# Optimization experiments

Measured on AMD Instinct MI355X. Metric: run time of the kernel, lower is better.

Reference implementation:

```python
import jax, jax.numpy as jnp
import numpy as np

N_WAY, K_SHOT = 5, 1
N_CLASSES = 64
D = 8


def _conv(x, w, b):
    y = jax.lax.conv_general_dilated(x, w, (2, 2), 'SAME',
                                     dimension_numbers=('NCHW', 'OIHW', 'NCHW'))
    return jax.nn.relu(y + b[None, :, None, None])


def setup_inputs() -> dict:
    key = jax.random.key(0)
    ks = jax.random.split(key, 12)
    b, s_sup, q, h, w = 4, N_WAY * K_SHOT, 1, 64, 64
    rnd = lambda k, shape: jax.random.normal(k, shape, jnp.float32) * 0.05
    return {
        'support_x': jax.random.normal(ks[0], (b, s_sup, 3, h, w), jnp.float32),
        'support_y': jax.random.randint(ks[1], (b, s_sup), 0, N_CLASSES),
        'query_x': jax.random.normal(ks[2], (b, q, 3, h, w), jnp.float32),
        'query_y': jax.random.randint(ks[3], (b, q), 0, N_CLASSES),
        'k1': rnd(ks[4], (32, 3, 3, 3)), 'bc1': jnp.zeros((32,), jnp.float32),
        'k2': rnd(ks[5], (48, 32, 3, 3)), 'bc2': jnp.zeros((48,), jnp.float32),
        'k3': rnd(ks[6], (64, 48, 3, 3)), 'bc3': jnp.zeros((64,), jnp.float32),
        'Wlog': rnd(ks[7], (64, N_CLASSES)), 'blog': jnp.zeros((N_CLASSES,), jnp.float32),
        'Wg1': rnd(ks[8], (132, 128)), 'bg1': jnp.zeros((128,), jnp.float32),
        'Wg2': rnd(ks[9], (128, 64)), 'bg2': jnp.zeros((64,), jnp.float32),
        'Wf1': rnd(ks[10], (64, 16)), 'bf1': jnp.zeros((16,), jnp.float32),
        'Wf2': rnd(ks[11], (16, 1)), 'bf2': jnp.zeros((1,), jnp.float32),
    }


def reference(support_x, support_y, query_x, query_y,
              k1, bc1, k2, bc2, k3, bc3, Wlog, blog,
              Wg1, bg1, Wg2, bg2, Wf1, bf1, Wf2, bf2):
    x = jnp.concatenate([support_x, query_x], axis=1)       # [b, s, 3, h, w]
    label = jnp.concatenate([support_y, query_y], axis=1)   # [b, s]
    b, s = label.shape
    h, w = x.shape[-2:]

    feat = x.reshape(b * s, 3, h, w)
    feat = _conv(feat, k1, bc1)
    feat = _conv(feat, k2, bc2)
    feat = _conv(feat, k3, bc3)                              # [b*s, c, D, D]
    c = feat.shape[1]
    logits = feat.mean(axis=(2, 3)) @ Wlog + blog            # [b*s, n_classes]

    # --- append normalized (i/d, j/d) coord channels ---
    ii = jnp.arange(D, dtype=feat.dtype) / D
    coord = jnp.stack([jnp.broadcast_to(ii[:, None], (D, D)),
                       jnp.broadcast_to(ii[None, :], (D, D))])        # [2, D, D]
    feat = feat.reshape(b, s, c, D, D)
    feat = jnp.concatenate([feat, jnp.broadcast_to(coord, (b, s, 2, D, D))], axis=2)
    c2 = c + 2
    m = D * D
    a = feat.reshape(b, s, c2, m).transpose(0, 1, 3, 2)      # [b, s, m, c2]

    # --- relation network g over all (set-pair, position-pair) combos ---
    # original: g(concat(x_i, x_j)) where x_i = x[b, j, :, q], x_j = x[b, i, :, p]
    # split first linear: concat @ Wg1 = x_i @ Wg1[:c2] + x_j @ Wg1[c2:]
    W1a, W1b = Wg1[:c2], Wg1[c2:]
    u = a @ W1a                                              # [b, s_j, m_q, 128]
    v = a @ W1b + bg1                                        # [b, s_i, m_p, 128]
    # hdd[b,i,j,q,p] = relu(u[b,j,q] + v[b,i,p])  -> [b, s, s, m, m, 128]
    hdd = jax.nn.relu(u[:, None, :, :, None, :] + v[:, :, None, None, :, :])
    g = jax.nn.relu(hdd @ Wg2 + bg2)                         # [b, s, s, m, m, 64]
    x_f = g.sum(axis=(3, 4))                                 # [b, s, s, 64]
    score = jax.nn.sigmoid(jax.nn.relu(x_f @ Wf1 + bf1) @ Wf2 + bf2)  # [b, s, s, 1]

    # --- losses ---
    logp = jax.nn.log_softmax(logits, axis=-1)
    lab = label.reshape(-1)
    cls_loss = -jnp.take_along_axis(logp, lab[:, None], axis=1).mean()

    y = (label[:, :, None] == label[:, None, :])[..., None].astype(score.dtype)
    P = score[..., 0]                                        # [b, s, s]
    Pt = P.transpose(0, 2, 1)
    sym, anti = 0.5 * (P + Pt), 0.5 * (P - Pt)
    sym_n = jnp.sqrt((sym ** 2).sum(axis=(1, 2)))            # Frobenius per batch
    anti_n = jnp.sqrt((anti ** 2).sum(axis=(1, 2)))
    sym_loss = ((sym_n - anti_n) / (sym_n + anti_n)).mean()
    euc_loss = ((score - y) ** 2).mean()
    rn_loss = euc_loss - 0.1 * sym_loss
    return (cls_loss, rn_loss, sym_loss)
```

## Files before the change

kernel.cpp:

```cpp
#include <hip/hip_runtime.h>

typedef _Float16 f16x8 __attribute__((ext_vector_type(8)));
typedef float f32x4 __attribute__((ext_vector_type(4)));


__global__ void conv1_k(const float* __restrict__ sx, const float* __restrict__ qx,
                        const float* __restrict__ w, const float* __restrict__ bias,
                        float* __restrict__ out,
                        const float* __restrict__ Wg2, _Float16* __restrict__ W2h) {
    if (blockIdx.x == 768) {
        for (int s = 0; s < 4; s++) {
            int slot = threadIdx.x + 256*s;
            int tile = slot >> 6, lane = slot & 63;
            int kt = tile >> 2, nt = tile & 3;
            int quad = lane >> 4, col = lane & 15;
            f16x8 t;
            #pragma unroll
            for (int jj = 0; jj < 8; jj++)
                t[jj] = (_Float16)Wg2[(kt*32 + quad*8 + jj)*64 + nt*16 + col];
            *(f16x8*)&W2h[slot*8] = t;
        }
        return;
    }
    int r8 = blockIdx.x & 7, q = blockIdx.x >> 3;
    int n  = (q >> 5)*8 + r8;
    int oc = q & 31;
    int bi = n / 6, si = n % 6;
    const float* inp = (si < 5) ? sx + (size_t)((bi*5+si)*3)*4096
                                : qx + (size_t)(bi*3)*4096;
    __shared__ float wl[27];
    __shared__ float bl;
    if (threadIdx.x < 27) wl[threadIdx.x] = w[oc*27 + threadIdx.x];
    if (threadIdx.x == 0) bl = bias[oc];
    __syncthreads();
    for (int idx = threadIdx.x; idx < 1024; idx += 256) {
        int oy = idx >> 5, ox = idx & 31;
        float acc = bl;
        #pragma unroll
        for (int ic = 0; ic < 3; ic++) {
            const float* ip = inp + ic*4096;
            #pragma unroll
            for (int dy = 0; dy < 3; dy++) {
                int iy = 2*oy + dy;
                if (iy >= 64) continue;
                #pragma unroll
                for (int dx = 0; dx < 3; dx++) {
                    int ix = 2*ox + dx;
                    if (ix >= 64) continue;
                    acc += ip[iy*64+ix] * wl[ic*9 + dy*3 + dx];
                }
            }
        }
        out[(size_t)(n*32+oc)*1024 + idx] = fmaxf(acc, 0.f);
    }
}

__global__ void conv2_k(const float* __restrict__ in, const float* __restrict__ w,
                        const float* __restrict__ bias, float* __restrict__ out) {
    int r8 = blockIdx.x & 7, q = blockIdx.x >> 3;
    int n   = (q / 12)*8 + r8;
    int ocg = q % 12;
    __shared__ float wl[1152];
    __shared__ float pin[3][33*32];
    const int tid = threadIdx.x;
    for (int e = tid; e < 1152; e += 256) wl[e] = w[ocg*1152 + e];
    const float* ib = in + (size_t)n*32*1024;
    int srow = (tid*4) >> 5, scol = (tid*4) & 31;
    {
        f32x4 t0 = *(const f32x4*)&ib[tid*4];
        float* d = &pin[0][srow*33 + scol];
        d[0]=t0[0]; d[1]=t0[1]; d[2]=t0[2]; d[3]=t0[3];
    }
    f32x4 t1 = *(const f32x4*)&ib[1024 + tid*4];
    __syncthreads();
    int oy = tid >> 4, ox = tid & 15;
    float a0 = bias[ocg*4+0], a1 = bias[ocg*4+1];
    float a2 = bias[ocg*4+2], a3 = bias[ocg*4+3];
    for (int ic = 0; ic < 32; ic++) {
        f32x4 t2 = t1;
        if (ic + 2 < 32) t2 = *(const f32x4*)&ib[(size_t)(ic+2)*1024 + tid*4];
        const float* pp = pin[ic % 3];
        float tap[9];
        #pragma unroll
        for (int dy = 0; dy < 3; dy++)
            #pragma unroll
            for (int dx = 0; dx < 3; dx++) {
                int iy = 2*oy+dy, ix = 2*ox+dx;
                tap[dy*3+dx] = (iy < 32 && ix < 32) ? pp[iy*33 + ix] : 0.f;
            }
        #pragma unroll
        for (int t = 0; t < 9; t++) {
            a0 += tap[t]*wl[0*288 + ic*9 + t];
            a1 += tap[t]*wl[1*288 + ic*9 + t];
            a2 += tap[t]*wl[2*288 + ic*9 + t];
            a3 += tap[t]*wl[3*288 + ic*9 + t];
        }
        if (ic + 1 < 32) {
            float* d = &pin[(ic+1) % 3][srow*33 + scol];
            d[0]=t1[0]; d[1]=t1[1]; d[2]=t1[2]; d[3]=t1[3];
        }
        t1 = t2;
        __syncthreads();
    }
    size_t ob = (size_t)(n*48 + ocg*4)*256 + tid;
    out[ob        ] = fmaxf(a0, 0.f);
    out[ob + 256  ] = fmaxf(a1, 0.f);
    out[ob + 512  ] = fmaxf(a2, 0.f);
    out[ob + 768  ] = fmaxf(a3, 0.f);
}

__global__ void conv3_k(const float* __restrict__ in, const float* __restrict__ w,
                        const float* __restrict__ bias, float* __restrict__ out,
                        float* __restrict__ mf) {
    int r8 = blockIdx.x & 7, q = blockIdx.x >> 3;
    int n   = (q >> 3)*8 + r8;
    int ocg = q & 7;
    __shared__ float wl[3456];
    __shared__ float pin[3][17*16];
    const int tid = threadIdx.x;
    for (int e = tid; e < 3456; e += 256) wl[e] = w[ocg*3456 + e];
    const float* ib = in + (size_t)n*48*256;
    int srow = tid >> 4, scol = tid & 15;
    pin[0][srow*17 + scol] = ib[tid];
    float t1 = ib[256 + tid];
    __syncthreads();
    int pix = tid & 63, osub = tid >> 6;
    int oy = pix >> 3, ox = pix & 7;
    int ol0 = osub*2;
    float a0 = bias[ocg*8 + ol0], a1 = bias[ocg*8 + ol0 + 1];
    for (int ic = 0; ic < 48; ic++) {
        float t2 = t1;
        if (ic + 2 < 48) t2 = ib[(size_t)(ic+2)*256 + tid];
        const float* pp = pin[ic % 3];
        float tap[9];
        #pragma unroll
        for (int dy = 0; dy < 3; dy++)
            #pragma unroll
            for (int dx = 0; dx < 3; dx++) {
                int iy = 2*oy+dy, ix = 2*ox+dx;
                tap[dy*3+dx] = (iy < 16 && ix < 16) ? pp[iy*17 + ix] : 0.f;
            }
        #pragma unroll
        for (int t = 0; t < 9; t++) {
            a0 += tap[t]*wl[ ol0   *432 + ic*9 + t];
            a1 += tap[t]*wl[(ol0+1)*432 + ic*9 + t];
        }
        if (ic + 1 < 48) pin[(ic+1) % 3][srow*17 + scol] = t1;
        t1 = t2;
        __syncthreads();
    }
    float r0 = fmaxf(a0, 0.f), r1 = fmaxf(a1, 0.f);
    out[(size_t)(n*64 + ocg*8 + ol0  )*64 + pix] = r0;
    out[(size_t)(n*64 + ocg*8 + ol0+1)*64 + pix] = r1;
    #pragma unroll
    for (int off = 32; off >= 1; off >>= 1) {
        r0 += __shfl_xor(r0, off, 64);
        r1 += __shfl_xor(r1, off, 64);
    }
    if (pix == 0) {
        mf[n*64 + ocg*8 + ol0    ] = r0 * (1.f/64.f);
        mf[n*64 + ocg*8 + ol0 + 1] = r1 * (1.f/64.f);
    }
}

__global__ void uvcls_k(const float* __restrict__ feat3, const float* __restrict__ Wg1,
                        const float* __restrict__ bg1, _Float16* __restrict__ u,
                        _Float16* __restrict__ v,
                        const float* __restrict__ mf, const int* __restrict__ sy,
                        const int* __restrict__ qy, const float* __restrict__ Wlog,
                        const float* __restrict__ blog, float* __restrict__ rv) {
    int tid = threadIdx.x;
    if (blockIdx.x >= 384) {
        int n = blockIdx.x - 384;
        if (tid >= 64) return;
        int lane = tid;
        float s = blog[lane];
        for (int c = 0; c < 64; c++) s += mf[n*64 + c] * Wlog[c*64 + lane];
        float mx = s;
        #pragma unroll
        for (int off = 32; off >= 1; off >>= 1) mx = fmaxf(mx, __shfl_xor(mx, off, 64));
        float p = __expf(s - mx);
        float se = p;
        #pragma unroll
        for (int off = 32; off >= 1; off >>= 1) se += __shfl_xor(se, off, 64);
        int bi = n/6, si = n%6;
        int lab = (si < 5) ? sy[bi*5+si] : qy[bi];
        float s_lab = __shfl(s, lab, 64);
        if (lane == 0) rv[n] = -(s_lab - mx - __logf(se));
        return;
    }
    int r8 = blockIdx.x & 7, q = blockIdx.x >> 3;
    int bs = (q >> 4)*8 + r8;
    int pg = q & 15;
    __shared__ float a4[4][66];
    for (int e = tid; e < 264; e += 128) {
        int pl = e / 66, c = e % 66;
        int p = pg*4 + pl;
        float vv;
        if (c < 64)       vv = feat3[(size_t)(bs*64 + c)*64 + p];
        else if (c == 64) vv = (float)(p >> 3) * 0.125f;
        else              vv = (float)(p & 7) * 0.125f;
        a4[pl][c] = vv;
    }
    __syncthreads();
    float us[4] = {0.f,0.f,0.f,0.f};
    float bg = bg1[tid];
    float vs[4] = {bg,bg,bg,bg};
    for (int c = 0; c < 66; c++) {
        float wa = Wg1[c*128 + tid];
        float wb = Wg1[(66+c)*128 + tid];
        #pragma unroll
        for (int pl = 0; pl < 4; pl++) {
            us[pl] += a4[pl][c]*wa;
            vs[pl] += a4[pl][c]*wb;
        }
    }
    #pragma unroll
    for (int pl = 0; pl < 4; pl++) {
        int p = pg*4 + pl;
        u[(size_t)(bs*64+p)*128 + tid] = (_Float16)us[pl];
        v[(size_t)(bs*64+p)*128 + tid] = (_Float16)vs[pl];
    }
}

__global__ void __launch_bounds__(256) rel_k(
        const _Float16* __restrict__ U, const _Float16* __restrict__ V,
        const _Float16* __restrict__ W2h, const float* __restrict__ bg2,
        float* __restrict__ xfpart) {
    __shared__ __align__(16) _Float16 Vsh[16*128];
    __shared__ float xfred[4][64];

    int r8 = blockIdx.x & 7, qq = blockIdx.x >> 3;
    int b = r8 >> 1;
    int m = (qq << 1) | (r8 & 1);
    int cb = m >> 2, qc = m & 3;
    int j = cb / 6, i = cb % 6;
    int tid  = threadIdx.x;
    int wv   = tid >> 6, lane = tid & 63;
    int col  = lane & 15, quad = lane >> 4;

    const _Float16* ub = U + (size_t)(b*6 + i)*8192;
    const _Float16* vb = V + (size_t)(b*6 + j)*8192 + qc*16*128;

    *(f16x8*)&Vsh[tid*8] = *(const f16x8*)&vb[tid*8];

    f16x8 uf[4];
    {
        const _Float16* up = ub + (wv*16 + col)*128 + quad*8;
        #pragma unroll
        for (int kt = 0; kt < 4; kt++) uf[kt] = *(const f16x8*)&up[kt*32];
    }
    f16x8 bf[4][4];
    #pragma unroll
    for (int kt = 0; kt < 4; kt++)
        #pragma unroll
        for (int nt = 0; nt < 4; nt++)
            bf[kt][nt] = *(const f16x8*)&W2h[(size_t)(((kt*4+nt)*64) + lane)*8];
    float bgv[4];
    #pragma unroll
    for (int nt = 0; nt < 4; nt++) bgv[nt] = bg2[nt*16 + col];

    __syncthreads();

    float sums[4] = {0.f,0.f,0.f,0.f};
    for (int q = 0; q < 16; q++) {
        const _Float16* vp = &Vsh[q*128 + quad*8];
        f32x4 acc[4];
        #pragma unroll
        for (int nt = 0; nt < 4; nt++)
            acc[nt] = (f32x4){bgv[nt], bgv[nt], bgv[nt], bgv[nt]};
        #pragma unroll
        for (int kt = 0; kt < 4; kt++) {
            f16x8 vf = *(const f16x8*)&vp[kt*32];
            f16x8 af = uf[kt] + vf;
            af = __builtin_elementwise_max(af, (f16x8){0,0,0,0,0,0,0,0});
            #pragma unroll
            for (int nt = 0; nt < 4; nt++)
                acc[nt] = __builtin_amdgcn_mfma_f32_16x16x32_f16(af, bf[kt][nt], acc[nt], 0, 0, 0);
        }
        #pragma unroll
        for (int nt = 0; nt < 4; nt++)
            #pragma unroll
            for (int rr = 0; rr < 4; rr++)
                sums[nt] += fmaxf(acc[nt][rr], 0.f);
    }

    #pragma unroll
    for (int nt = 0; nt < 4; nt++) {
        sums[nt] += __shfl_xor(sums[nt], 16, 64);
        sums[nt] += __shfl_xor(sums[nt], 32, 64);
    }
    if (lane < 16) {
        #pragma unroll
        for (int nt = 0; nt < 4; nt++) xfred[wv][nt*16 + lane] = sums[nt];
    }
    __syncthreads();
    if (tid < 64)
        xfpart[(size_t)(b*144 + m)*64 + tid] =
            xfred[0][tid] + xfred[1][tid] + xfred[2][tid] + xfred[3][tid];
}

__global__ void loss_k(const float* __restrict__ xfp, const float* __restrict__ rv,
                       const int* __restrict__ sy, const int* __restrict__ qy,
                       const float* __restrict__ Wf1, const float* __restrict__ bf1,
                       const float* __restrict__ Wf2, const float* __restrict__ bf2,
                       float* __restrict__ out) {
    __shared__ float Wf1sh[1024];
    __shared__ float wf2sh[16];
    __shared__ float bf1sh[16];
    __shared__ float Pm[144];
    __shared__ int lab[24];
    __shared__ float red[256];
    __shared__ float ratio[4];
    int tid = threadIdx.x;
    for (int e = tid; e < 1024; e += 256) Wf1sh[e] = Wf1[e];
    if (tid < 16) { wf2sh[tid] = Wf2[tid]; bf1sh[tid] = bf1[tid]; }
    if (tid < 24) { int bi = tid/6, si = tid%6; lab[tid] = (si < 5) ? sy[bi*5+si] : qy[bi]; }
    __syncthreads();
    if (tid < 144) {
        float hid[16];
        #pragma unroll
        for (int h = 0; h < 16; h++) hid[h] = bf1sh[h];
        const float* xb = xfp + (size_t)tid*4*64;
        for (int n = 0; n < 64; n++) {
            float x = xb[n] + xb[64+n] + xb[128+n] + xb[192+n];
            #pragma unroll
            for (int h = 0; h < 16; h++) hid[h] += x * Wf1sh[n*16 + h];
        }
        float sc = bf2[0];
        #pragma unroll
        for (int h = 0; h < 16; h++) sc += fmaxf(hid[h], 0.f) * wf2sh[h];
        Pm[tid] = 1.f/(1.f + __expf(-sc));
    }
    __syncthreads();
    float e = 0.f;
    if (tid < 144) {
        int b = tid/36, r = tid%36, jj = r/6, ii = r%6;
        float y = (lab[b*6+jj] == lab[b*6+ii]) ? 1.f : 0.f;
        float d = Pm[tid] - y;
        e = d*d;
    }
    red[tid] = e;
    __syncthreads();
    for (int s = 128; s > 0; s >>= 1) {
        if (tid < s) red[tid] += red[tid+s];
        __syncthreads();
    }
    if (tid < 4) {
        float s2 = 0.f, a2 = 0.f;
        for (int jj = 0; jj < 6; jj++)
            for (int ii = 0; ii < 6; ii++) {
                float pa = Pm[tid*36 + jj*6 + ii], pb = Pm[tid*36 + ii*6 + jj];
                float sm = 0.5f*(pa+pb), an = 0.5f*(pa-pb);
                s2 += sm*sm; a2 += an*an;
            }
        float sn = sqrtf(s2), anq = sqrtf(a2);
        ratio[tid] = (sn - anq)/(sn + anq);
    }
    __syncthreads();
    if (tid == 0) {
        float sl = 0.25f*(ratio[0]+ratio[1]+ratio[2]+ratio[3]);
        float euc = red[0] * (1.f/144.f);
        float cs = 0.f;
        for (int k = 0; k < 24; k++) cs += rv[k];
        out[0] = cs * (1.f/24.f);
        out[1] = euc - 0.1f*sl;
        out[2] = sl;
    }
}

extern "C" void kernel_launch(void* const* d_in, const int* in_sizes, int n_in,
                              void* d_out, int out_size, void* d_ws, size_t ws_size,
                              hipStream_t stream) {
    const float* sx   = (const float*)d_in[0];
    const int*   sy   = (const int*)  d_in[1];
    const float* qx   = (const float*)d_in[2];
    const int*   qy   = (const int*)  d_in[3];
    const float* k1   = (const float*)d_in[4];
    const float* bc1  = (const float*)d_in[5];
    const float* k2   = (const float*)d_in[6];
    const float* bc2  = (const float*)d_in[7];
    const float* k3   = (const float*)d_in[8];
    const float* bc3  = (const float*)d_in[9];
    const float* Wlog = (const float*)d_in[10];
    const float* blog = (const float*)d_in[11];
    const float* Wg1  = (const float*)d_in[12];
    const float* bg1  = (const float*)d_in[13];
    const float* Wg2  = (const float*)d_in[14];
    const float* bg2  = (const float*)d_in[15];
    const float* Wf1  = (const float*)d_in[16];
    const float* bf1  = (const float*)d_in[17];
    const float* Wf2  = (const float*)d_in[18];
    const float* bf2  = (const float*)d_in[19];

    float* ws    = (float*)d_ws;
    float* feat1 = ws;
    float* feat2 = feat1 + 786432;
    float* feat3 = feat2 + 294912;
    float* mf    = feat3 + 98304;
    float* rv    = mf    + 1536;
    float* xfp   = rv    + 32;
    _Float16* u16 = (_Float16*)(xfp + 36864);
    _Float16* v16 = u16 + 196608;
    _Float16* W2h = v16 + 196608;
    float* out   = (float*)d_out;

    conv1_k <<<769,    256, 0, stream>>>(sx, qx, k1, bc1, feat1, Wg2, W2h);
    conv2_k <<<24*12,  256, 0, stream>>>(feat1, k2, bc2, feat2);
    conv3_k <<<24*8,   256, 0, stream>>>(feat2, k3, bc3, feat3, mf);
    uvcls_k <<<408,    128, 0, stream>>>(feat3, Wg1, bg1, u16, v16,
                                         mf, sy, qy, Wlog, blog, rv);
    rel_k   <<<576,    256, 0, stream>>>(u16, v16, W2h, bg2, xfp);
    loss_k  <<<1,      256, 0, stream>>>(xfp, rv, sy, qy, Wf1, bf1, Wf2, bf2, out);
}
```

Before: 178.5 us.

## Stage conv inputs fully in LDS and fuse loss into rel kernel via last-block atomic

conv1 now stages the whole 3-channel input image in padded shared memory instead of reading taps from global memory. conv2 and conv3 load all (or half) of their input planes up front with vector loads, which removes the per-channel rotating buffer and its per-iteration barriers. The loss kernel is folded into rel_k: the last block to finish, found with a global atomic counter, computes the losses, and xfpart is stored transposed so that block can read it with vector loads. The intent is to cut global-memory latency, barrier count and one kernel launch, at the cost of much more LDS per block (lower occupancy) and a persistent device counter that relies on the modulo-576 trick.

New measurement: 179.1 us. No clear change (+0.3%).

```diff
diff --git a/kernel.cpp b/kernel.cpp
--- a/kernel.cpp
+++ b/kernel.cpp
@@ -3,11 +3,14 @@
 typedef _Float16 f16x8 __attribute__((ext_vector_type(8)));
 typedef float f32x4 __attribute__((ext_vector_type(4)));
 
-
-__global__ void conv1_k(const float* __restrict__ sx, const float* __restrict__ qx,
-                        const float* __restrict__ w, const float* __restrict__ bias,
-                        float* __restrict__ out,
-                        const float* __restrict__ Wg2, _Float16* __restrict__ W2h) {
+__device__ unsigned g_rel_done = 0;
+
+
+__global__ void __launch_bounds__(256) conv1_k(
+        const float* __restrict__ sx, const float* __restrict__ qx,
+        const float* __restrict__ w, const float* __restrict__ bias,
+        float* __restrict__ out,
+        const float* __restrict__ Wg2, _Float16* __restrict__ W2h) {
     if (blockIdx.x == 768) {
         for (int s = 0; s < 4; s++) {
             int slot = threadIdx.x + 256*s;
@@ -28,17 +31,26 @@
     int bi = n / 6, si = n % 6;
     const float* inp = (si < 5) ? sx + (size_t)((bi*5+si)*3)*4096
                                 : qx + (size_t)(bi*3)*4096;
+    __shared__ __align__(16) float ish[3*4352];
     __shared__ float wl[27];
     __shared__ float bl;
-    if (threadIdx.x < 27) wl[threadIdx.x] = w[oc*27 + threadIdx.x];
-    if (threadIdx.x == 0) bl = bias[oc];
-    __syncthreads();
-    for (int idx = threadIdx.x; idx < 1024; idx += 256) {
+    const int tid = threadIdx.x;
+    #pragma unroll
+    for (int j = 0; j < 12; j++) {
+        int k = tid + j*256;
+        f32x4 t = *(const f32x4*)&inp[k*4];
+        int plane = k >> 10, rem = k & 1023, row = rem >> 4, c4 = (rem & 15)*4;
+        *(f32x4*)&ish[plane*4352 + row*68 + c4] = t;
+    }
+    if (tid < 27) wl[tid] = w[oc*27 + tid];
+    if (tid == 31) bl = bias[oc];
+    __syncthreads();
+    for (int idx = tid; idx < 1024; idx += 256) {
         int oy = idx >> 5, ox = idx & 31;
         float acc = bl;
         #pragma unroll
         for (int ic = 0; ic < 3; ic++) {
-            const float* ip = inp + ic*4096;
+            const float* ip = &ish[ic*4352];
             #pragma unroll
             for (int dy = 0; dy < 3; dy++) {
                 int iy = 2*oy + dy;
@@ -47,7 +59,7 @@
                 for (int dx = 0; dx < 3; dx++) {
                     int ix = 2*ox + dx;
                     if (ix >= 64) continue;
-                    acc += ip[iy*64+ix] * wl[ic*9 + dy*3 + dx];
+                    acc += ip[iy*68+ix] * wl[ic*9 + dy*3 + dx];
                 }
             }
         }
@@ -55,38 +67,45 @@
     }
 }
 
-__global__ void conv2_k(const float* __restrict__ in, const float* __restrict__ w,
-                        const float* __restrict__ bias, float* __restrict__ out) {
+__global__ void __launch_bounds__(256) conv2_k(
+        const float* __restrict__ in, const float* __restrict__ w,
+        const float* __restrict__ bias, float* __restrict__ out) {
     int r8 = blockIdx.x & 7, q = blockIdx.x >> 3;
     int n   = (q / 12)*8 + r8;
     int ocg = q % 12;
-    __shared__ float wl[1152];
-    __shared__ float pin[3][33*32];
+    __shared__ __align__(16) float wl[1152];
+    __shared__ __align__(16) float pin[16*1152];
     const int tid = threadIdx.x;
-    for (int e = tid; e < 1152; e += 256) wl[e] = w[ocg*1152 + e];
     const float* ib = in + (size_t)n*32*1024;
-    int srow = (tid*4) >> 5, scol = (tid*4) & 31;
-    {
-        f32x4 t0 = *(const f32x4*)&ib[tid*4];
-        float* d = &pin[0][srow*33 + scol];
-        d[0]=t0[0]; d[1]=t0[1]; d[2]=t0[2]; d[3]=t0[3];
-    }
-    f32x4 t1 = *(const f32x4*)&ib[1024 + tid*4];
+    #pragma unroll
+    for (int j = 0; j < 16; j++) {
+        int k = tid + j*256;
+        f32x4 t = *(const f32x4*)&ib[k*4];
+        int s = k >> 8, rem = k & 255, row = rem >> 3, c4 = (rem & 7)*4;
+        *(f32x4*)&pin[s*1152 + row*36 + c4] = t;
+    }
+    f32x4 rb[16];
+    #pragma unroll
+    for (int j = 0; j < 16; j++) {
+        int k = tid + j*256;
+        rb[j] = *(const f32x4*)&ib[16384 + k*4];
+    }
+    for (int e = tid; e < 288; e += 256)
+        *(f32x4*)&wl[e*4] = *(const f32x4*)&w[ocg*1152 + e*4];
     __syncthreads();
     int oy = tid >> 4, ox = tid & 15;
     float a0 = bias[ocg*4+0], a1 = bias[ocg*4+1];
     float a2 = bias[ocg*4+2], a3 = bias[ocg*4+3];
-    for (int ic = 0; ic < 32; ic++) {
-        f32x4 t2 = t1;
-        if (ic + 2 < 32) t2 = *(const f32x4*)&ib[(size_t)(ic+2)*1024 + tid*4];
-        const float* pp = pin[ic % 3];
+    #pragma unroll 4
+    for (int ic = 0; ic < 16; ic++) {
+        const float* pp = &pin[ic*1152];
         float tap[9];
         #pragma unroll
         for (int dy = 0; dy < 3; dy++)
             #pragma unroll
             for (int dx = 0; dx < 3; dx++) {
                 int iy = 2*oy+dy, ix = 2*ox+dx;
-                tap[dy*3+dx] = (iy < 32 && ix < 32) ? pp[iy*33 + ix] : 0.f;
+                tap[dy*3+dx] = (iy < 32 && ix < 32) ? pp[iy*36 + ix] : 0.f;
             }
         #pragma unroll
         for (int t = 0; t < 9; t++) {
@@ -95,12 +114,33 @@
             a2 += tap[t]*wl[2*288 + ic*9 + t];
             a3 += tap[t]*wl[3*288 + ic*9 + t];
         }
-        if (ic + 1 < 32) {
-            float* d = &pin[(ic+1) % 3][srow*33 + scol];
-            d[0]=t1[0]; d[1]=t1[1]; d[2]=t1[2]; d[3]=t1[3];
-        }
-        t1 = t2;
-        __syncthreads();
+    }
+    __syncthreads();
+    #pragma unroll
+    for (int j = 0; j < 16; j++) {
+        int k = tid + j*256;
+        int s = k >> 8, rem = k & 255, row = rem >> 3, c4 = (rem & 7)*4;
+        *(f32x4*)&pin[s*1152 + row*36 + c4] = rb[j];
+    }
+    __syncthreads();
+    #pragma unroll 4
+    for (int ic = 16; ic < 32; ic++) {
+        const float* pp = &pin[(ic-16)*1152];
+        float tap[9];
+        #pragma unroll
+        for (int dy = 0; dy < 3; dy++)
+            #pragma unroll
+            for (int dx = 0; dx < 3; dx++) {
+                int iy = 2*oy+dy, ix = 2*ox+dx;
+                tap[dy*3+dx] = (iy < 32 && ix < 32) ? pp[iy*36 + ix] : 0.f;
+            }
+        #pragma unroll
+        for (int t = 0; t < 9; t++) {
+            a0 += tap[t]*wl[0*288 + ic*9 + t];
+            a1 += tap[t]*wl[1*288 + ic*9 + t];
+            a2 += tap[t]*wl[2*288 + ic*9 + t];
+            a3 += tap[t]*wl[3*288 + ic*9 + t];
+        }
     }
     size_t ob = (size_t)(n*48 + ocg*4)*256 + tid;
     out[ob        ] = fmaxf(a0, 0.f);
@@ -109,45 +149,47 @@
     out[ob + 768  ] = fmaxf(a3, 0.f);
 }
 
-__global__ void conv3_k(const float* __restrict__ in, const float* __restrict__ w,
-                        const float* __restrict__ bias, float* __restrict__ out,
-                        float* __restrict__ mf) {
+__global__ void __launch_bounds__(256) conv3_k(
+        const float* __restrict__ in, const float* __restrict__ w,
+        const float* __restrict__ bias, float* __restrict__ out,
+        float* __restrict__ mf) {
     int r8 = blockIdx.x & 7, q = blockIdx.x >> 3;
     int n   = (q >> 3)*8 + r8;
     int ocg = q & 7;
-    __shared__ float wl[3456];
-    __shared__ float pin[3][17*16];
+    __shared__ __align__(16) float wl[3456];
+    __shared__ __align__(16) float pin[48*320];
     const int tid = threadIdx.x;
-    for (int e = tid; e < 3456; e += 256) wl[e] = w[ocg*3456 + e];
     const float* ib = in + (size_t)n*48*256;
-    int srow = tid >> 4, scol = tid & 15;
-    pin[0][srow*17 + scol] = ib[tid];
-    float t1 = ib[256 + tid];
+    #pragma unroll
+    for (int j = 0; j < 12; j++) {
+        int k = tid + j*256;
+        f32x4 t = *(const f32x4*)&ib[k*4];
+        int plane = k >> 6, rem = k & 63, row = rem >> 2, c4 = (rem & 3)*4;
+        *(f32x4*)&pin[plane*320 + row*20 + c4] = t;
+    }
+    for (int e = tid; e < 864; e += 256)
+        *(f32x4*)&wl[e*4] = *(const f32x4*)&w[ocg*3456 + e*4];
     __syncthreads();
     int pix = tid & 63, osub = tid >> 6;
     int oy = pix >> 3, ox = pix & 7;
     int ol0 = osub*2;
     float a0 = bias[ocg*8 + ol0], a1 = bias[ocg*8 + ol0 + 1];
+    #pragma unroll 4
     for (int ic = 0; ic < 48; ic++) {
-        float t2 = t1;
-        if (ic + 2 < 48) t2 = ib[(size_t)(ic+2)*256 + tid];
-        const float* pp = pin[ic % 3];
+        const float* pp = &pin[ic*320];
         float tap[9];
         #pragma unroll
         for (int dy = 0; dy < 3; dy++)
             #pragma unroll
             for (int dx = 0; dx < 3; dx++) {
                 int iy = 2*oy+dy, ix = 2*ox+dx;
-                tap[dy*3+dx] = (iy < 16 && ix < 16) ? pp[iy*17 + ix] : 0.f;
+                tap[dy*3+dx] = (iy < 16 && ix < 16) ? pp[iy*20 + ix] : 0.f;
             }
         #pragma unroll
         for (int t = 0; t < 9; t++) {
             a0 += tap[t]*wl[ ol0   *432 + ic*9 + t];
             a1 += tap[t]*wl[(ol0+1)*432 + ic*9 + t];
         }
-        if (ic + 1 < 48) pin[(ic+1) % 3][srow*17 + scol] = t1;
-        t1 = t2;
-        __syncthreads();
     }
     float r0 = fmaxf(a0, 0.f), r1 = fmaxf(a1, 0.f);
     out[(size_t)(n*64 + ocg*8 + ol0  )*64 + pix] = r0;
@@ -226,9 +268,16 @@
 __global__ void __launch_bounds__(256) rel_k(
         const _Float16* __restrict__ U, const _Float16* __restrict__ V,
         const _Float16* __restrict__ W2h, const float* __restrict__ bg2,
-        float* __restrict__ xfpart) {
-    __shared__ __align__(16) _Float16 Vsh[16*128];
-    __shared__ float xfred[4][64];
+        float* __restrict__ xfpT,
+        const float* __restrict__ rv,
+        const int* __restrict__ sy, const int* __restrict__ qy,
+        const float* __restrict__ Wf1, const float* __restrict__ bf1,
+        const float* __restrict__ Wf2, const float* __restrict__ bf2,
+        float* __restrict__ out) {
+    __shared__ __align__(16) float smem[1792];
+    __shared__ unsigned lastflag;
+    _Float16* Vsh   = (_Float16*)smem;
+    float*    xfred = smem + 1024;
 
     int r8 = blockIdx.x & 7, qq = blockIdx.x >> 3;
     int b = r8 >> 1;
@@ -263,8 +312,8 @@
     __syncthreads();
 
     float sums[4] = {0.f,0.f,0.f,0.f};
-    for (int q = 0; q < 16; q++) {
-        const _Float16* vp = &Vsh[q*128 + quad*8];
+    for (int qi = 0; qi < 16; qi++) {
+        const _Float16* vp = &Vsh[qi*128 + quad*8];
         f32x4 acc[4];
         #pragma unroll
         for (int nt = 0; nt < 4; nt++)
@@ -292,80 +341,89 @@
     }
     if (lane < 16) {
         #pragma unroll
-        for (int nt = 0; nt < 4; nt++) xfred[wv][nt*16 + lane] = sums[nt];
+        for (int nt = 0; nt < 4; nt++) xfred[wv*64 + nt*16 + lane] = sums[nt];
     }
     __syncthreads();
     if (tid < 64)
-        xfpart[(size_t)(b*144 + m)*64 + tid] =
-            xfred[0][tid] + xfred[1][tid] + xfred[2][tid] + xfred[3][tid];
-}
-
-__global__ void loss_k(const float* __restrict__ xfp, const float* __restrict__ rv,
-                       const int* __restrict__ sy, const int* __restrict__ qy,
-                       const float* __restrict__ Wf1, const float* __restrict__ bf1,
-                       const float* __restrict__ Wf2, const float* __restrict__ bf2,
-                       float* __restrict__ out) {
-    __shared__ float Wf1sh[1024];
-    __shared__ float wf2sh[16];
-    __shared__ float bf1sh[16];
-    __shared__ float Pm[144];
-    __shared__ int lab[24];
-    __shared__ float red[256];
-    __shared__ float ratio[4];
-    int tid = threadIdx.x;
-    for (int e = tid; e < 1024; e += 256) Wf1sh[e] = Wf1[e];
-    if (tid < 16) { wf2sh[tid] = Wf2[tid]; bf1sh[tid] = bf1[tid]; }
-    if (tid < 24) { int bi = tid/6, si = tid%6; lab[tid] = (si < 5) ? sy[bi*5+si] : qy[bi]; }
-    __syncthreads();
-    if (tid < 144) {
-        float hid[16];
-        #pragma unroll
-        for (int h = 0; h < 16; h++) hid[h] = bf1sh[h];
-        const float* xb = xfp + (size_t)tid*4*64;
-        for (int n = 0; n < 64; n++) {
-            float x = xb[n] + xb[64+n] + xb[128+n] + xb[192+n];
-            #pragma unroll
-            for (int h = 0; h < 16; h++) hid[h] += x * Wf1sh[n*16 + h];
-        }
-        float sc = bf2[0];
-        #pragma unroll
-        for (int h = 0; h < 16; h++) sc += fmaxf(hid[h], 0.f) * wf2sh[h];
-        Pm[tid] = 1.f/(1.f + __expf(-sc));
-    }
-    __syncthreads();
-    float e = 0.f;
-    if (tid < 144) {
-        int b = tid/36, r = tid%36, jj = r/6, ii = r%6;
-        float y = (lab[b*6+jj] == lab[b*6+ii]) ? 1.f : 0.f;
-        float d = Pm[tid] - y;
-        e = d*d;
-    }
-    red[tid] = e;
-    __syncthreads();
-    for (int s = 128; s > 0; s >>= 1) {
-        if (tid < s) red[tid] += red[tid+s];
+        xfpT[(size_t)tid*576 + (unsigned)(b*144 + m)] =
+            xfred[tid] + xfred[64+tid] + xfred[128+tid] + xfred[192+tid];
+
+    __syncthreads();
+    if (tid == 0) {
+        __threadfence();
+        unsigned my = __hip_atomic_fetch_add(&g_rel_done, 1u, __ATOMIC_ACQ_REL,
+                                             __HIP_MEMORY_SCOPE_AGENT);
+        lastflag = ((my % 576u) == 575u) ? 1u : 0u;
+    }
+    __syncthreads();
+    if (!lastflag) return;
+    if (tid == 0)
+        (void)__hip_atomic_load(&g_rel_done, __ATOMIC_ACQUIRE,
+                                __HIP_MEMORY_SCOPE_AGENT);
+    __syncthreads();
+
+    {
+        float* Wf1sh = smem;
+        float* wf2sh = smem + 1024;
+        float* bf1sh = smem + 1040;
+        float* Pm    = smem + 1056;
+        int*   lab   = (int*)(smem + 1200);
+        float* red   = smem + 1232;
+        float* ratio = smem + 1488;
+        for (int e = tid; e < 1024; e += 256) Wf1sh[e] = Wf1[e];
+        if (tid < 16) { wf2sh[tid] = Wf2[tid]; bf1sh[tid] = bf1[tid]; }
+        if (tid < 24) { int bi = tid/6, si = tid%6; lab[tid] = (si < 5) ? sy[bi*5+si] : qy[bi]; }
         __syncthreads();
-    }
-    if (tid < 4) {
-        float s2 = 0.f, a2 = 0.f;
-        for (int jj = 0; jj < 6; jj++)
-            for (int ii = 0; ii < 6; ii++) {
-                float pa = Pm[tid*36 + jj*6 + ii], pb = Pm[tid*36 + ii*6 + jj];
-                float sm = 0.5f*(pa+pb), an = 0.5f*(pa-pb);
-                s2 += sm*sm; a2 += an*an;
+        if (tid < 144) {
+            float hid[16];
+            #pragma unroll
+            for (int h = 0; h < 16; h++) hid[h] = bf1sh[h];
+            for (int nn = 0; nn < 64; nn++) {
+                f32x4 vv = *(const f32x4*)&xfpT[(size_t)nn*576 + tid*4];
+                float x = vv[0] + vv[1] + vv[2] + vv[3];
+                #pragma unroll
+                for (int h = 0; h < 16; h++) hid[h] += x * Wf1sh[nn*16 + h];
             }
-        float sn = sqrtf(s2), anq = sqrtf(a2);
-        ratio[tid] = (sn - anq)/(sn + anq);
-    }
-    __syncthreads();
-    if (tid == 0) {
-        float sl = 0.25f*(ratio[0]+ratio[1]+ratio[2]+ratio[3]);
-        float euc = red[0] * (1.f/144.f);
-        float cs = 0.f;
-        for (int k = 0; k < 24; k++) cs += rv[k];
-        out[0] = cs * (1.f/24.f);
-        out[1] = euc - 0.1f*sl;
-        out[2] = sl;
+            float sc = bf2[0];
+            #pragma unroll
+            for (int h = 0; h < 16; h++) sc += fmaxf(hid[h], 0.f) * wf2sh[h];
+            Pm[tid] = 1.f/(1.f + __expf(-sc));
+        }
+        __syncthreads();
+        float e = 0.f;
+        if (tid < 144) {
+            int bb = tid/36, r = tid%36, jj = r/6, ii = r%6;
+            float y = (lab[bb*6+jj] == lab[bb*6+ii]) ? 1.f : 0.f;
+            float d = Pm[tid] - y;
+            e = d*d;
+        }
+        red[tid] = e;
+        __syncthreads();
+        for (int s = 128; s > 0; s >>= 1) {
+            if (tid < s) red[tid] += red[tid+s];
+            __syncthreads();
+        }
+        if (tid < 4) {
+            float s2 = 0.f, a2 = 0.f;
+            for (int jj = 0; jj < 6; jj++)
+                for (int ii = 0; ii < 6; ii++) {
+                    float pa = Pm[tid*36 + jj*6 + ii], pb = Pm[tid*36 + ii*6 + jj];
+                    float sm = 0.5f*(pa+pb), an = 0.5f*(pa-pb);
+                    s2 += sm*sm; a2 += an*an;
+                }
+            float sn = sqrtf(s2), anq = sqrtf(a2);
+            ratio[tid] = (sn - anq)/(sn + anq);
+        }
+        __syncthreads();
+        if (tid == 0) {
+            float sl = 0.25f*(ratio[0]+ratio[1]+ratio[2]+ratio[3]);
+            float euc = red[0] * (1.f/144.f);
+            float cs = 0.f;
+            for (int k = 0; k < 24; k++) cs += rv[k];
+            out[0] = cs * (1.f/24.f);
+            out[1] = euc - 0.1f*sl;
+            out[2] = sl;
+        }
     }
 }
 
@@ -399,8 +457,8 @@
     float* feat3 = feat2 + 294912;
     float* mf    = feat3 + 98304;
     float* rv    = mf    + 1536;
-    float* xfp   = rv    + 32;
-    _Float16* u16 = (_Float16*)(xfp + 36864);
+    float* xfpT  = rv    + 32;
+    _Float16* u16 = (_Float16*)(xfpT + 36864);
     _Float16* v16 = u16 + 196608;
     _Float16* W2h = v16 + 196608;
     float* out   = (float*)d_out;
@@ -410,6 +468,6 @@
     conv3_k <<<24*8,   256, 0, stream>>>(feat2, k3, bc3, feat3, mf);
     uvcls_k <<<408,    128, 0, stream>>>(feat3, Wg1, bg1, u16, v16,
                                          mf, sy, qy, Wlog, blog, rv);
-    rel_k   <<<576,    256, 0, stream>>>(u16, v16, W2h, bg2, xfp);
-    loss_k  <<<1,      256, 0, stream>>>(xfp, rv, sy, qy, Wf1, bf1, Wf2, bf2, out);
-}
+    rel_k   <<<576,    256, 0, stream>>>(u16, v16, W2h, bg2, xfpT,
+                                         rv, sy, qy, Wf1, bf1, Wf2, bf2, out);
+}
```
